# Kernel optimization log

Measured on AMD Instinct MI355X. Metric: run time of the kernel, lower is better.

## Reference

```python
import jax, jax.numpy as jnp
import numpy as np

BS, LX, LY, D, H, DK = 2, 2048, 2048, 1024, 16, 64


def setup_inputs() -> dict:
    key = jax.random.key(0)
    ks = jax.random.split(key, 12)
    s = 1.0 / np.sqrt(D)
    return {
        "x": jax.random.normal(ks[0], (BS, LX, D), jnp.float32),
        "y": jax.random.normal(ks[1], (BS, LY, D), jnp.float32),
        "mask": jnp.zeros((BS, 1, LX, LY), jnp.float32),
        "Wq": jax.random.normal(ks[2], (D, H * DK), jnp.float32) * s,
        "bq": jnp.zeros((H * DK,), jnp.float32),
        "Wk": jax.random.normal(ks[3], (D, H * DK), jnp.float32) * s,
        "bk": jnp.zeros((H * DK,), jnp.float32),
        "Wv": jax.random.normal(ks[4], (D, H * DK), jnp.float32) * s,
        "bv": jnp.zeros((H * DK,), jnp.float32),
        "Wo": jax.random.normal(ks[5], (H * DK, D), jnp.float32) * s,
        "bo": jnp.zeros((D,), jnp.float32),
    }


def reference(x, y, mask, Wq, bq, Wk, bk, Wv, bv, Wo, bo):
    bs, lx, _ = x.shape
    ly = y.shape[1]
    norm = DK ** 0.5
    # projections -> (bs, len, H, DK)
    q = (x @ Wq + bq).reshape(bs, lx, H, DK)
    k = (y @ Wk + bk).reshape(bs, ly, H, DK)
    v = (y @ Wv + bv).reshape(bs, ly, H, DK)
    # scores: (bs, H, lx, ly)
    scores = jnp.einsum('bxhd,byhd->bhxy', q, k) / norm + mask
    attn = jax.nn.softmax(scores, axis=-1)
    # output: (bs, lx, H, DK) -> (bs, lx, H*DK)
    out = jnp.einsum('bhxy,byhd->bxhd', attn, v).reshape(bs, lx, H * DK)
    return out @ Wo + bo
```

## Files before the change

kernel.cpp:

```cpp
#include <hip/hip_runtime.h>
#include <hip/hip_bf16.h>


typedef __bf16 bf16;
typedef __bf16 bf16x4 __attribute__((ext_vector_type(4)));
typedef __bf16 bf16x8 __attribute__((ext_vector_type(8)));
typedef float floatx4 __attribute__((ext_vector_type(4)));

#define MFMA16(a, b, c) __builtin_amdgcn_mfma_f32_16x16x32_bf16(a, b, c, 0, 0, 0)

constexpr int BS = 2, LX = 2048, LY = 2048, D = 1024, H = 16, DK = 64;
constexpr int HD = H * DK;
constexpr float LOG2E = 1.4426950408889634f;

__device__ __forceinline__ void cp16(const bf16* g, bf16* l) {
  __builtin_amdgcn_global_load_lds(
      (const __attribute__((address_space(1))) unsigned int*)g,
      (__attribute__((address_space(3))) unsigned int*)l, 16, 0, 0);
}

__global__ __launch_bounds__(256) void prep(const float* __restrict__ W0, bf16* __restrict__ T0,
                                            const float* __restrict__ W1, bf16* __restrict__ T1,
                                            const float* __restrict__ W2, bf16* __restrict__ T2,
                                            const float* __restrict__ W3, bf16* __restrict__ T3,
                                            const float* __restrict__ x, bf16* __restrict__ xb,
                                            const float* __restrict__ y, bf16* __restrict__ yb,
                                            const float* __restrict__ mask, int* __restrict__ flags) {
  const int id = blockIdx.x;
  const int t = threadIdx.x;
  if (id < 1024) {
    __shared__ bf16 tile[64][72];
    const float* W;
    bf16* T;
    switch (id >> 8) {
      case 0: W = W0; T = T0; break;
      case 1: W = W1; T = T1; break;
      case 2: W = W2; T = T2; break;
      default: W = W3; T = T3; break;
    }
    const int kt = id & 15, nt = (id >> 4) & 15;
    const int r = t >> 2, c4 = (t & 3) * 16;
    const float* src = W + (size_t)(kt * 64 + r) * 1024 + nt * 64 + c4;
#pragma unroll
    for (int i = 0; i < 16; i++) tile[r][c4 + i] = (bf16)src[i];
    __syncthreads();
    bf16 vals[16];
#pragma unroll
    for (int i = 0; i < 16; i++) vals[i] = tile[c4 + i][r];
    bf16* dst = T + (size_t)(nt * 64 + r) * 1024 + kt * 64 + c4;
#pragma unroll
    for (int i = 0; i < 16; i++) dst[i] = vals[i];
  } else if (id < 5120) {
    const int id2 = id - 1024;
    const float* src = (id2 >= 2048) ? y : x;
    bf16* dst = (id2 >= 2048) ? yb : xb;
    const size_t i = ((size_t)(id2 & 2047) * 256 + t) * 8;
    float4 a = *(const float4*)(src + i);
    float4 c = *(const float4*)(src + i + 4);
    bf16 tmp[8] = {(bf16)a.x, (bf16)a.y, (bf16)a.z, (bf16)a.w,
                   (bf16)c.x, (bf16)c.y, (bf16)c.z, (bf16)c.w};
    *(bf16x8*)(dst + i) = *(const bf16x8*)tmp;
  } else {
    const int id3 = id - 5120;
    const int region = id3 >> 5, sub = id3 & 31;
    const float4* p = (const float4*)mask + (size_t)region * 65536 + sub * 2048;
    bool nz = false;
#pragma unroll
    for (int it = 0; it < 8; it++) {
      float4 v = p[it * 256 + t];
      nz |= (v.x != 0.f) | (v.y != 0.f) | (v.z != 0.f) | (v.w != 0.f);
    }
    if (nz) atomicOr(&flags[region], 1);
  }
}

__global__ __launch_bounds__(256) void qkv_gemm(const bf16* __restrict__ xb, const bf16* __restrict__ yb,
                                                const bf16* __restrict__ Wtq, const bf16* __restrict__ Wtk,
                                                const bf16* __restrict__ Wtv,
                                                const float* __restrict__ bq, const float* __restrict__ bk,
                                                const float* __restrict__ bv,
                                                bf16* __restrict__ Qb, bf16* __restrict__ Kb,
                                                bf16* __restrict__ Vt) {
  constexpr int K = 1024, N = 1024;
  __shared__ __align__(16) bf16 smem[128 * 136];
  bf16* As = smem;
  bf16* Bs = smem + 128 * 64;
  bf16* Ct = smem;

  const int z = blockIdx.z;
  const bf16* A = (z == 0) ? xb : yb;
  const bf16* Bt = (z == 0) ? Wtq : (z == 1) ? Wtk : Wtv;
  const float* bias = (z == 0) ? bq : (z == 1) ? bk : bv;

  const int t = threadIdx.x;
  const int w = t >> 6, lane = t & 63, quad = lane >> 4, l15 = lane & 15;
  const int wr = (w & 1) * 64, wc = (w >> 1) * 64;
  const int mbase = blockIdx.y * 128, nbase = blockIdx.x * 128;
  const int srow = lane >> 3, schunk = (lane & 7) ^ srow;
  const int sx = quad ^ (l15 & 7);

  floatx4 acc[4][4] = {};

  for (int k0 = 0; k0 < K; k0 += 64) {
    __syncthreads();
#pragma unroll
    for (int j = 0; j < 4; j++) {
      const int r0 = w * 32 + j * 8;
      cp16(A + (size_t)(mbase + r0 + srow) * K + k0 + schunk * 8, As + r0 * 64);
      cp16(Bt + (size_t)(nbase + r0 + srow) * K + k0 + schunk * 8, Bs + r0 * 64);
    }
    __syncthreads();
    bf16x8 af[4][2], bfr[4][2];
#pragma unroll
    for (int i = 0; i < 4; i++) {
      const int ra = wr + i * 16 + l15;
      af[i][0] = *(const bf16x8*)&As[ra * 64 + sx * 8];
      af[i][1] = *(const bf16x8*)&As[ra * 64 + (sx ^ 4) * 8];
      const int rb = wc + i * 16 + l15;
      bfr[i][0] = *(const bf16x8*)&Bs[rb * 64 + sx * 8];
      bfr[i][1] = *(const bf16x8*)&Bs[rb * 64 + (sx ^ 4) * 8];
    }
#pragma unroll
    for (int i = 0; i < 4; i++)
#pragma unroll
      for (int jn = 0; jn < 4; jn++) {
        acc[i][jn] = MFMA16(af[i][0], bfr[jn][0], acc[i][jn]);
        acc[i][jn] = MFMA16(af[i][1], bfr[jn][1], acc[i][jn]);
      }
  }

  if (z <= 1) {
    bf16* outp = (z == 0) ? Qb : Kb;
    const float sc = (z == 0) ? 0.125f * LOG2E : 1.0f;
#pragma unroll
    for (int jn = 0; jn < 4; jn++) {
      const int n = nbase + wc + jn * 16 + l15;
      const float bv2 = bias[n];
#pragma unroll
      for (int i = 0; i < 4; i++)
#pragma unroll
        for (int r = 0; r < 4; r++) {
          const int m = mbase + wr + i * 16 + quad * 4 + r;
          outp[(size_t)m * N + n] = (bf16)((acc[i][jn][r] + bv2) * sc);
        }
    }
  } else {
    __syncthreads();
#pragma unroll
    for (int jn = 0; jn < 4; jn++) {
      const int nl = wc + jn * 16 + l15;
      const float bv2 = bias[nbase + nl];
#pragma unroll
      for (int i = 0; i < 4; i++)
#pragma unroll
        for (int r = 0; r < 4; r++) {
          const int ml = wr + i * 16 + quad * 4 + r;
          Ct[nl * 136 + ml] = (bf16)(acc[i][jn][r] + bv2);
        }
    }
    __syncthreads();
    const int n = t >> 1, mh = (t & 1) * 64;
    const int gn = nbase + n;
    const int hh = gn >> 6, dk = gn & 63;
    const int bb = mbase >> 11, y0 = (mbase & 2047) + mh;
    bf16* dst = Vt + ((size_t)(bb * H + hh) * DK + dk) * LY + y0;
    const bf16* srcr = &Ct[n * 136 + mh];
#pragma unroll
    for (int u = 0; u < 8; u++) *(bf16x8*)(dst + u * 8) = *(const bf16x8*)(srcr + u * 8);
  }
}

__global__ __launch_bounds__(256) void out_gemm(const bf16* __restrict__ A, const bf16* __restrict__ Bt,
                                                const float* __restrict__ bias, float* __restrict__ outp) {
  constexpr int K = 1024, N = 1024;
  __shared__ __align__(16) bf16 As[128 * 64];
  __shared__ __align__(16) bf16 Bs[64 * 64];
  const int t = threadIdx.x;
  const int w = t >> 6, lane = t & 63, quad = lane >> 4, l15 = lane & 15;
  const int mbase = blockIdx.y * 128, nbase = blockIdx.x * 64;
  const int srow = lane >> 3, schunk = (lane & 7) ^ srow;
  const int sx = quad ^ (l15 & 7);

  floatx4 acc[2][4] = {};
  for (int k0 = 0; k0 < K; k0 += 64) {
    __syncthreads();
#pragma unroll
    for (int j = 0; j < 4; j++) {
      const int r0 = w * 32 + j * 8;
      cp16(A + (size_t)(mbase + r0 + srow) * K + k0 + schunk * 8, As + r0 * 64);
    }
#pragma unroll
    for (int j = 0; j < 2; j++) {
      const int r0 = w * 16 + j * 8;
      cp16(Bt + (size_t)(nbase + r0 + srow) * K + k0 + schunk * 8, Bs + r0 * 64);
    }
    __syncthreads();
    bf16x8 af[2][2], bfr[4][2];
#pragma unroll
    for (int i = 0; i < 2; i++) {
      const int ra = w * 32 + i * 16 + l15;
      af[i][0] = *(const bf16x8*)&As[ra * 64 + sx * 8];
      af[i][1] = *(const bf16x8*)&As[ra * 64 + (sx ^ 4) * 8];
    }
#pragma unroll
    for (int jn = 0; jn < 4; jn++) {
      const int rb = jn * 16 + l15;
      bfr[jn][0] = *(const bf16x8*)&Bs[rb * 64 + sx * 8];
      bfr[jn][1] = *(const bf16x8*)&Bs[rb * 64 + (sx ^ 4) * 8];
    }
#pragma unroll
    for (int i = 0; i < 2; i++)
#pragma unroll
      for (int jn = 0; jn < 4; jn++) {
        acc[i][jn] = MFMA16(af[i][0], bfr[jn][0], acc[i][jn]);
        acc[i][jn] = MFMA16(af[i][1], bfr[jn][1], acc[i][jn]);
      }
  }
#pragma unroll
  for (int jn = 0; jn < 4; jn++) {
    const int n = nbase + jn * 16 + l15;
    const float bv2 = bias[n];
#pragma unroll
    for (int i = 0; i < 2; i++)
#pragma unroll
      for (int r = 0; r < 4; r++) {
        const int m = mbase + w * 32 + i * 16 + quad * 4 + r;
        outp[(size_t)m * N + n] = acc[i][jn][r] + bv2;
      }
  }
}

__global__ __launch_bounds__(256) void attn7(const bf16* __restrict__ Q, const bf16* __restrict__ Kb,
                                             const bf16* __restrict__ Vt, const float* __restrict__ mask,
                                             const int* __restrict__ flags, bf16* __restrict__ OP,
                                             float* __restrict__ LP) {
  __shared__ __align__(16) bf16 Ks[2][64 * 64];
  __shared__ __align__(16) bf16 Vs[2][64 * 64];
  __shared__ __align__(16) bf16 Plds[4][32 * 72];
  const int t = threadIdx.x;
  const int w = t >> 6, lane = t & 63, quad = lane >> 4, l15 = lane & 15;
  const int xt = blockIdx.x, h = blockIdx.y;
  const int b = blockIdx.z >> 1, split = blockIdx.z & 1;
  const int qbase = xt * 128 + w * 32;
  const int y0 = split * 1024;
  const int srow = lane >> 3, schunk = (lane & 7) ^ srow;
  const int sx = quad ^ (l15 & 7);

  bf16x8 qf[2][2];
#pragma unroll
  for (int rt = 0; rt < 2; rt++) {
    const bf16* qrow = Q + (size_t)(b * LX + qbase + rt * 16 + l15) * HD + h * DK;
    qf[rt][0] = *(const bf16x8*)(qrow + quad * 8);
    qf[rt][1] = *(const bf16x8*)(qrow + 32 + quad * 8);
  }
  const int mflag = flags[b * 16 + xt];

  bf16 onearr[8];
#pragma unroll
  for (int i = 0; i < 8; i++) onearr[i] = (bf16)((l15 == 0) ? 1.0f : 0.0f);
  const bf16x8 onesf = *(const bf16x8*)onearr;

  floatx4 o[2][4] = {};
  floatx4 ol[2] = {};

  const bf16* Kbase = Kb + (size_t)(b * LY + y0) * HD + h * DK;
  const bf16* Vbase = Vt + (size_t)(b * H + h) * DK * LY + y0;
  const float* mbase2 = mask + (size_t)(b * LX + qbase + l15) * LY + y0;

#define STAGE(yt, bufi)                                                               \
  {                                                                                   \
    _Pragma("unroll") for (int j = 0; j < 2; j++) {                                   \
      const int r0 = w * 16 + j * 8;                                                  \
      cp16(Kbase + (size_t)((yt) + r0 + srow) * HD + schunk * 8, &Ks[bufi][r0 * 64]); \
      cp16(Vbase + (size_t)(r0 + srow) * LY + (yt) + schunk * 8, &Vs[bufi][r0 * 64]); \
    }                                                                                 \
  }

#define TILE(yt, BUF)                                                                       \
  {                                                                                         \
    const bf16* KsB = Ks[BUF];                                                              \
    const bf16* VsB = Vs[BUF];                                                              \
    bf16x8 kf[4][2];                                                                        \
    _Pragma("unroll") for (int nt = 0; nt < 4; nt++) {                                      \
      const int ry = nt * 16 + l15;                                                         \
      kf[nt][0] = *(const bf16x8*)&KsB[ry * 64 + sx * 8];                                   \
      kf[nt][1] = *(const bf16x8*)&KsB[ry * 64 + (sx ^ 4) * 8];                             \
    }                                                                                       \
    floatx4 s[2][4] = {};                                                                   \
    _Pragma("unroll") for (int nt = 0; nt < 4; nt++)                                        \
        _Pragma("unroll") for (int rt = 0; rt < 2; rt++) {                                  \
      s[rt][nt] = MFMA16(kf[nt][0], qf[rt][0], s[rt][nt]);                                  \
      s[rt][nt] = MFMA16(kf[nt][1], qf[rt][1], s[rt][nt]);                                  \
    }                                                                                       \
    if (mflag) {                                                                            \
      _Pragma("unroll") for (int rt = 0; rt < 2; rt++)                                      \
          _Pragma("unroll") for (int nt = 0; nt < 4; nt++) {                                \
        const float* mp = mbase2 + (size_t)rt * 16 * LY + (yt) + nt * 16 + quad * 4;        \
        float4 mv = *(const float4*)mp;                                                     \
        s[rt][nt][0] = fminf(s[rt][nt][0] + LOG2E * mv.x, 30.f);                            \
        s[rt][nt][1] = fminf(s[rt][nt][1] + LOG2E * mv.y, 30.f);                            \
        s[rt][nt][2] = fminf(s[rt][nt][2] + LOG2E * mv.z, 30.f);                            \
        s[rt][nt][3] = fminf(s[rt][nt][3] + LOG2E * mv.w, 30.f);                            \
      }                                                                                     \
    }                                                                                       \
    _Pragma("unroll") for (int rt = 0; rt < 2; rt++)                                        \
        _Pragma("unroll") for (int nt = 0; nt < 4; nt++) {                                  \
      bf16x4 pk;                                                                            \
      _Pragma("unroll") for (int r = 0; r < 4; r++)                                         \
          pk[r] = (bf16)__builtin_amdgcn_exp2f(s[rt][nt][r]);                               \
      *(bf16x4*)&Plds[w][(rt * 16 + l15) * 72 + nt * 16 + quad * 4] = pk;                   \
    }                                                                                       \
    bf16x8 pf[2][2];                                                                        \
    _Pragma("unroll") for (int rt = 0; rt < 2; rt++) {                                      \
      const bf16* prow = &Plds[w][(rt * 16 + l15) * 72];                                    \
      pf[rt][0] = *(const bf16x8*)(prow + quad * 8);                                        \
      pf[rt][1] = *(const bf16x8*)(prow + 32 + quad * 8);                                   \
    }                                                                                       \
    _Pragma("unroll") for (int u = 0; u < 4; u++) {                                         \
      const int rd = u * 16 + l15;                                                          \
      bf16x8 v0 = *(const bf16x8*)&VsB[rd * 64 + sx * 8];                                   \
      bf16x8 v1 = *(const bf16x8*)&VsB[rd * 64 + (sx ^ 4) * 8];                             \
      _Pragma("unroll") for (int rt = 0; rt < 2; rt++) {                                    \
        o[rt][u] = MFMA16(pf[rt][0], v0, o[rt][u]);                                         \
        o[rt][u] = MFMA16(pf[rt][1], v1, o[rt][u]);                                         \
      }                                                                                     \
    }                                                                                       \
    _Pragma("unroll") for (int rt = 0; rt < 2; rt++) {                                      \
      ol[rt] = MFMA16(pf[rt][0], onesf, ol[rt]);                                            \
      ol[rt] = MFMA16(pf[rt][1], onesf, ol[rt]);                                            \
    }                                                                                       \
  }

  STAGE(0, 0);
  for (int yt = 0; yt < 1024; yt += 128) {
    __syncthreads();
    STAGE(yt + 64, 1);
    TILE(yt, 0);
    __syncthreads();
    if (yt + 128 < 1024) STAGE(yt + 128, 0);
    TILE(yt + 64, 1);
  }

  bf16* OPp = OP + (size_t)split * BS * LX * HD;
  float* LPp = LP + (size_t)split * BS * H * LX;
#pragma unroll
  for (int rt = 0; rt < 2; rt++) {
#pragma unroll
    for (int r = 0; r < 4; r++) {
      const int m = b * LX + qbase + rt * 16 + quad * 4 + r;
#pragma unroll
      for (int u = 0; u < 4; u++)
        OPp[(size_t)m * HD + h * DK + u * 16 + l15] = (bf16)o[rt][u][r];
    }
    if (l15 == 0)
      *(floatx4*)&LPp[(size_t)(b * H + h) * LX + qbase + rt * 16 + quad * 4] = ol[rt];
  }
#undef STAGE
#undef TILE
}

__global__ __launch_bounds__(256) void hmerge(const bf16* __restrict__ OP, const float* __restrict__ LP,
                                              bf16* __restrict__ Hb) {
  const size_t i8 = ((size_t)blockIdx.x * 256 + threadIdx.x) * 8;
  const bf16x8 a = *(const bf16x8*)(OP + i8);
  const bf16x8 b = *(const bf16x8*)(OP + (size_t)BS * LX * HD + i8);
  const int bb = (int)(i8 >> 21);
  const int x = (int)(i8 >> 10) & 2047;
  const int h = (int)(i8 >> 6) & 15;
  const size_t li = (size_t)(bb * H + h) * LX + x;
  const float rl = 1.0f / (LP[li] + LP[(size_t)BS * H * LX + li]);
  bf16 outv[8];
#pragma unroll
  for (int j = 0; j < 8; j++) outv[j] = (bf16)(((float)a[j] + (float)b[j]) * rl);
  *(bf16x8*)(Hb + i8) = *(const bf16x8*)outv;
}

extern "C" void kernel_launch(void* const* d_in, const int* in_sizes, int n_in,
                              void* d_out, int out_size, void* d_ws, size_t ws_size,
                              hipStream_t stream) {
  const float* x = (const float*)d_in[0];
  const float* y = (const float*)d_in[1];
  const float* mask = (const float*)d_in[2];
  const float* Wq = (const float*)d_in[3];
  const float* bq = (const float*)d_in[4];
  const float* Wk = (const float*)d_in[5];
  const float* bk = (const float*)d_in[6];
  const float* Wv = (const float*)d_in[7];
  const float* bv = (const float*)d_in[8];
  const float* Wo = (const float*)d_in[9];
  const float* bo = (const float*)d_in[10];

  char* ws = (char*)d_ws;
  size_t off = 0;
  int* flags = (int*)(ws + off); off += 256;
  bf16* Qb = (bf16*)(ws + off); off += (size_t)BS * LX * HD * 2;
  bf16* Kb = (bf16*)(ws + off); off += (size_t)BS * LY * HD * 2;
  bf16* Vt = (bf16*)(ws + off); off += (size_t)BS * LY * HD * 2;
  bf16* Hb = (bf16*)(ws + off); off += (size_t)BS * LX * HD * 2;
  const size_t region = off;
  bf16* xbf = (bf16*)(ws + off); off += (size_t)BS * LX * D * 2;
  bf16* ybf = (bf16*)(ws + off); off += (size_t)BS * LY * D * 2;
  bf16* Wtq = (bf16*)(ws + off); off += (size_t)D * HD * 2;
  bf16* Wtk = (bf16*)(ws + off); off += (size_t)D * HD * 2;
  bf16* Wtv = (bf16*)(ws + off); off += (size_t)D * HD * 2;
  bf16* Wto = (bf16*)(ws + off); off += (size_t)HD * D * 2;
  bf16* OP = (bf16*)(ws + region);
  float* LP = (float*)(ws + region + (size_t)2 * BS * LX * HD * 2);

  dim3 blk(256);
  hipMemsetAsync(flags, 0, 32 * sizeof(int), stream);
  prep<<<dim3(6144), blk, 0, stream>>>(Wq, Wtq, Wk, Wtk, Wv, Wtv, Wo, Wto, x, xbf, y, ybf, mask, flags);
  qkv_gemm<<<dim3(8, 32, 3), blk, 0, stream>>>(xbf, ybf, Wtq, Wtk, Wtv, bq, bk, bv, Qb, Kb, Vt);
  attn7<<<dim3(16, 16, 4), blk, 0, stream>>>(Qb, Kb, Vt, mask, flags, OP, LP);
  hmerge<<<dim3(2048), blk, 0, stream>>>(OP, LP, Hb);
  out_gemm<<<dim3(16, 32), blk, 0, stream>>>(Hb, Wto, bo, (float*)d_out);
}
```

Before: 248.9 us.

## Drop key-split in attention and fuse normalization, removing merge kernel

The attention kernel now processes the full key length per block instead of splitting it in two. It normalizes the output in-register using the row sum from the ones-MFMA column, broadcast by a shuffle. This removes the partial output/sum buffers and the separate merge kernel along with their global memory traffic and launch. The cost is half as many blocks and longer per-block loops, which reduces parallelism and latency hiding. A launch bound hint of 2 blocks per CU is added.

```diff
diff --git a/kernel.cpp b/kernel.cpp
--- a/kernel.cpp
+++ b/kernel.cpp
@@ -230,19 +230,16 @@
   }
 }
 
-__global__ __launch_bounds__(256) void attn7(const bf16* __restrict__ Q, const bf16* __restrict__ Kb,
-                                             const bf16* __restrict__ Vt, const float* __restrict__ mask,
-                                             const int* __restrict__ flags, bf16* __restrict__ OP,
-                                             float* __restrict__ LP) {
+__global__ __launch_bounds__(256, 2) void attn8(const bf16* __restrict__ Q, const bf16* __restrict__ Kb,
+                                                const bf16* __restrict__ Vt, const float* __restrict__ mask,
+                                                const int* __restrict__ flags, bf16* __restrict__ Hout) {
   __shared__ __align__(16) bf16 Ks[2][64 * 64];
   __shared__ __align__(16) bf16 Vs[2][64 * 64];
   __shared__ __align__(16) bf16 Plds[4][32 * 72];
   const int t = threadIdx.x;
   const int w = t >> 6, lane = t & 63, quad = lane >> 4, l15 = lane & 15;
-  const int xt = blockIdx.x, h = blockIdx.y;
-  const int b = blockIdx.z >> 1, split = blockIdx.z & 1;
+  const int xt = blockIdx.x, h = blockIdx.y, b = blockIdx.z;
   const int qbase = xt * 128 + w * 32;
-  const int y0 = split * 1024;
   const int srow = lane >> 3, schunk = (lane & 7) ^ srow;
   const int sx = quad ^ (l15 & 7);
 
@@ -263,9 +260,9 @@
   floatx4 o[2][4] = {};
   floatx4 ol[2] = {};
 
-  const bf16* Kbase = Kb + (size_t)(b * LY + y0) * HD + h * DK;
-  const bf16* Vbase = Vt + (size_t)(b * H + h) * DK * LY + y0;
-  const float* mbase2 = mask + (size_t)(b * LX + qbase + l15) * LY + y0;
+  const bf16* Kbase = Kb + (size_t)b * LY * HD + h * DK;
+  const bf16* Vbase = Vt + (size_t)(b * H + h) * DK * LY;
+  const float* mbase2 = mask + (size_t)(b * LX + qbase + l15) * LY;
 
 #define STAGE(yt, bufi)                                                               \
   {                                                                                   \
@@ -332,47 +329,28 @@
   }
 
   STAGE(0, 0);
-  for (int yt = 0; yt < 1024; yt += 128) {
+  for (int yt = 0; yt < LY; yt += 128) {
     __syncthreads();
     STAGE(yt + 64, 1);
     TILE(yt, 0);
     __syncthreads();
-    if (yt + 128 < 1024) STAGE(yt + 128, 0);
+    if (yt + 128 < LY) STAGE(yt + 128, 0);
     TILE(yt + 64, 1);
   }
 
-  bf16* OPp = OP + (size_t)split * BS * LX * HD;
-  float* LPp = LP + (size_t)split * BS * H * LX;
-#pragma unroll
-  for (int rt = 0; rt < 2; rt++) {
+#pragma unroll
+  for (int rt = 0; rt < 2; rt++)
 #pragma unroll
     for (int r = 0; r < 4; r++) {
+      const float lsum = __shfl(ol[rt][r], lane & 48, 64);
+      const float rl = 1.0f / lsum;
       const int m = b * LX + qbase + rt * 16 + quad * 4 + r;
 #pragma unroll
       for (int u = 0; u < 4; u++)
-        OPp[(size_t)m * HD + h * DK + u * 16 + l15] = (bf16)o[rt][u][r];
-    }
-    if (l15 == 0)
-      *(floatx4*)&LPp[(size_t)(b * H + h) * LX + qbase + rt * 16 + quad * 4] = ol[rt];
-  }
+        Hout[(size_t)m * HD + h * DK + u * 16 + l15] = (bf16)(o[rt][u][r] * rl);
+    }
 #undef STAGE
 #undef TILE
-}
-
-__global__ __launch_bounds__(256) void hmerge(const bf16* __restrict__ OP, const float* __restrict__ LP,
-                                              bf16* __restrict__ Hb) {
-  const size_t i8 = ((size_t)blockIdx.x * 256 + threadIdx.x) * 8;
-  const bf16x8 a = *(const bf16x8*)(OP + i8);
-  const bf16x8 b = *(const bf16x8*)(OP + (size_t)BS * LX * HD + i8);
-  const int bb = (int)(i8 >> 21);
-  const int x = (int)(i8 >> 10) & 2047;
-  const int h = (int)(i8 >> 6) & 15;
-  const size_t li = (size_t)(bb * H + h) * LX + x;
-  const float rl = 1.0f / (LP[li] + LP[(size_t)BS * H * LX + li]);
-  bf16 outv[8];
-#pragma unroll
-  for (int j = 0; j < 8; j++) outv[j] = (bf16)(((float)a[j] + (float)b[j]) * rl);
-  *(bf16x8*)(Hb + i8) = *(const bf16x8*)outv;
 }
 
 extern "C" void kernel_launch(void* const* d_in, const int* in_sizes, int n_in,
@@ -397,21 +375,17 @@
   bf16* Kb = (bf16*)(ws + off); off += (size_t)BS * LY * HD * 2;
   bf16* Vt = (bf16*)(ws + off); off += (size_t)BS * LY * HD * 2;
   bf16* Hb = (bf16*)(ws + off); off += (size_t)BS * LX * HD * 2;
-  const size_t region = off;
   bf16* xbf = (bf16*)(ws + off); off += (size_t)BS * LX * D * 2;
   bf16* ybf = (bf16*)(ws + off); off += (size_t)BS * LY * D * 2;
   bf16* Wtq = (bf16*)(ws + off); off += (size_t)D * HD * 2;
   bf16* Wtk = (bf16*)(ws + off); off += (size_t)D * HD * 2;
   bf16* Wtv = (bf16*)(ws + off); off += (size_t)D * HD * 2;
   bf16* Wto = (bf16*)(ws + off); off += (size_t)HD * D * 2;
-  bf16* OP = (bf16*)(ws + region);
-  float* LP = (float*)(ws + region + (size_t)2 * BS * LX * HD * 2);
 
   dim3 blk(256);
   hipMemsetAsync(flags, 0, 32 * sizeof(int), stream);
   prep<<<dim3(6144), blk, 0, stream>>>(Wq, Wtq, Wk, Wtk, Wv, Wtv, Wo, Wto, x, xbf, y, ybf, mask, flags);
   qkv_gemm<<<dim3(8, 32, 3), blk, 0, stream>>>(xbf, ybf, Wtq, Wtk, Wtv, bq, bk, bv, Qb, Kb, Vt);
-  attn7<<<dim3(16, 16, 4), blk, 0, stream>>>(Qb, Kb, Vt, mask, flags, OP, LP);
-  hmerge<<<dim3(2048), blk, 0, stream>>>(OP, LP, Hb);
+  attn8<<<dim3(16, 16, 2), blk, 0, stream>>>(Qb, Kb, Vt, mask, flags, Hb);
   out_gemm<<<dim3(16, 32), blk, 0, stream>>>(Hb, Wto, bo, (float*)d_out);
 }
```

Measured after the change: 238.8 us. -4.1%, faster.
